# Kernel tuning notes

Hardware: AMD Instinct MI355X
Metric: run time of the kernel (lower is better)

Reference implementation:

```python
import jax, jax.numpy as jnp
import numpy as np

B, DE, T = 32, 256, 32
H, W, C = 128, 128, 128  # units == C


def setup_inputs() -> dict:
    key = jax.random.key(0)
    k1, k2, k3 = jax.random.split(key, 3)
    e = jax.random.normal(k1, (B, DE, T), dtype=jnp.float32)
    h = jax.random.normal(k2, (B, H, W, C), dtype=jnp.float32)
    Wd = jax.random.normal(k3, (DE, C), dtype=jnp.float32) * (1.0 / np.sqrt(DE))
    b = jnp.zeros((C,), dtype=jnp.float32)
    return {"e": e, "h": h, "Wd": Wd, "b": b}


def reference(e, h, Wd, b):
    # e: [B, DE, T]  -> dense over DE -> e_: [B, C, T]
    e_ = jnp.einsum('bdt,dc->bct', e, Wd) + b[None, :, None]
    Bh, Hh, Wh, Ch = h.shape
    HW = Hh * Wh
    # h NHWC -> [B, C, HW]
    h1 = h.transpose(0, 3, 1, 2).reshape(Bh, Ch, HW)
    # scores: [B, T, HW], contraction over channels
    s = jnp.einsum('bct,bcn->btn', e_, h1)
    # softmax over T (axis=1)
    beta = jax.nn.softmax(s, axis=1)
    # context: [B, C, HW]
    c = jnp.einsum('bct,btn->bcn', e_, beta)
    # -> [B, HW, C] -> NHWC
    c = c.transpose(0, 2, 1).reshape(Bh, Hh, Wh, Ch)
    return jnp.concatenate([c, h], axis=3)  # [B, H, W, 2C]
```

## Files before the change

kernel.cpp:

```cpp
#include <hip/hip_runtime.h>

typedef float v2f __attribute__((ext_vector_type(2)));

#define B_   32
#define DE_  256
#define T_   32
#define C_   128
#define HW_  16384

#define HSTRIDE 257

__device__ inline v2f vfma2(v2f a, v2f b, v2f c) {
#if __has_builtin(__builtin_elementwise_fma)
    return __builtin_elementwise_fma(a, b, c);
#else
    v2f r; r.x = fmaf(a.x, b.x, c.x); r.y = fmaf(a.y, b.y, c.y); return r;
#endif
}

__global__ __launch_bounds__(256) void dense_e_kernel(
    const float* __restrict__ e, const float* __restrict__ Wd,
    const float* __restrict__ bias, float* __restrict__ ews)
{
    __shared__ float elds[DE_ * T_];
    __shared__ float wlds[DE_ * 16];
    const int b   = blockIdx.y;
    const int cq  = blockIdx.x;
    const int tid = threadIdx.x;

    {
        const float4* erow = (const float4*)(e + ((size_t)b * DE_ + tid) * T_);
        float4* edst = (float4*)(elds + tid * T_);
        #pragma unroll
        for (int i = 0; i < 8; ++i) edst[i] = erow[i];

        const float4* wrow = (const float4*)(Wd + (size_t)tid * C_ + cq * 16);
        float4* wdst = (float4*)(wlds + tid * 16);
        #pragma unroll
        for (int i = 0; i < 4; ++i) wdst[i] = wrow[i];
    }
    __syncthreads();

    const int t  = tid & 31;
    const int c8 = tid >> 5;
    float a0 = 0.f, a1 = 0.f;
    #pragma unroll 8
    for (int d = 0; d < DE_; ++d) {
        float ev = elds[d * T_ + t];
        a0 = fmaf(ev, wlds[d * 16 + c8],     a0);
        a1 = fmaf(ev, wlds[d * 16 + 8 + c8], a1);
    }
    const int c0 = cq * 16 + c8;
    a0 += bias[c0];
    a1 += bias[c0 + 8];
    ews[((size_t)b * C_ + c0)     * T_ + t] = a0;
    ews[((size_t)b * C_ + c0 + 8) * T_ + t] = a1;
}

__global__ __launch_bounds__(128) void attn_fused_kernel(
    const float* __restrict__ h,
    const float* __restrict__ ews,
    float* __restrict__ out)
{
    __shared__ float hT[16 * HSTRIDE];
    __shared__ float es[16 * T_];

    const int b   = blockIdx.x >> 6;
    const int n0  = (blockIdx.x & 63) << 8;
    const int tid = threadIdx.x;
    const float* __restrict__ eb = ews + (size_t)b * (C_ * T_);
    const float* __restrict__ hb = h   + ((size_t)b * HW_ + n0) * C_;
    float* __restrict__       ob = out + ((size_t)b * HW_ + n0) * (2 * C_);

    v2f s0[16], s1[16];
    #pragma unroll
    for (int i = 0; i < 16; ++i) { s0[i] = (v2f){0.f, 0.f}; s1[i] = (v2f){0.f, 0.f}; }

    for (int ch = 0; ch < 8; ++ch) {
        float4 hv[8];
        #pragma unroll
        for (int i = 0; i < 8; ++i) {
            const int idx = i * 128 + tid;
            hv[i] = *(const float4*)(hb + (size_t)(idx >> 2) * C_ + ch * 16 + (idx & 3) * 4);
        }
        ((float4*)es)[tid] = ((const float4*)(eb + ch * 16 * T_))[tid];
        #pragma unroll
        for (int i = 0; i < 8; ++i) {
            const int idx = i * 128 + tid;
            const int row = idx >> 2, c4 = idx & 3;
            *(float4*)(ob + (size_t)row * (2 * C_) + C_ + ch * 16 + c4 * 4) = hv[i];
            float* d = hT + (c4 * 4) * HSTRIDE + row;
            d[0]           = hv[i].x;
            d[HSTRIDE]     = hv[i].y;
            d[2 * HSTRIDE] = hv[i].z;
            d[3 * HSTRIDE] = hv[i].w;
        }
        __syncthreads();

        #pragma unroll
        for (int cl = 0; cl < 16; ++cl) {
            const float h0 = hT[cl * HSTRIDE + tid];
            const float h1 = hT[cl * HSTRIDE + 128 + tid];
            const float4* ec4 = (const float4*)(es + cl * T_);
            const v2f h0v = {h0, h0}, h1v = {h1, h1};
            #pragma unroll
            for (int k = 0; k < 8; ++k) {
                const float4 ef = ec4[k];
                const v2f eA = {ef.x, ef.y}, eB = {ef.z, ef.w};
                s0[2 * k]     = vfma2(h0v, eA, s0[2 * k]);
                s0[2 * k + 1] = vfma2(h0v, eB, s0[2 * k + 1]);
                s1[2 * k]     = vfma2(h1v, eA, s1[2 * k]);
                s1[2 * k + 1] = vfma2(h1v, eB, s1[2 * k + 1]);
            }
        }
        __syncthreads();
    }

    {
        v2f m2 = s0[0];
        #pragma unroll
        for (int i = 1; i < 16; ++i) { m2.x = fmaxf(m2.x, s0[i].x); m2.y = fmaxf(m2.y, s0[i].y); }
        const float m = fmaxf(m2.x, m2.y);
        float l = 0.f;
        #pragma unroll
        for (int i = 0; i < 16; ++i) {
            v2f p; p.x = __expf(s0[i].x - m); p.y = __expf(s0[i].y - m);
            s0[i] = p; l += p.x + p.y;
        }
        const float inv = 1.0f / l;
        #pragma unroll
        for (int i = 0; i < 16; ++i) { s0[i].x *= inv; s0[i].y *= inv; }
    }
    {
        v2f m2 = s1[0];
        #pragma unroll
        for (int i = 1; i < 16; ++i) { m2.x = fmaxf(m2.x, s1[i].x); m2.y = fmaxf(m2.y, s1[i].y); }
        const float m = fmaxf(m2.x, m2.y);
        float l = 0.f;
        #pragma unroll
        for (int i = 0; i < 16; ++i) {
            v2f p; p.x = __expf(s1[i].x - m); p.y = __expf(s1[i].y - m);
            s1[i] = p; l += p.x + p.y;
        }
        const float inv = 1.0f / l;
        #pragma unroll
        for (int i = 0; i < 16; ++i) { s1[i].x *= inv; s1[i].y *= inv; }
    }

    for (int ch = 0; ch < 8; ++ch) {
        ((float4*)es)[tid] = ((const float4*)(eb + ch * 16 * T_))[tid];
        __syncthreads();
        #pragma unroll
        for (int cl = 0; cl < 16; ++cl) {
            const float4* ec4 = (const float4*)(es + cl * T_);
            v2f a0 = {0.f, 0.f}, a1 = {0.f, 0.f};
            #pragma unroll
            for (int k = 0; k < 8; ++k) {
                const float4 ef = ec4[k];
                const v2f eA = {ef.x, ef.y}, eB = {ef.z, ef.w};
                a0 = vfma2(eA, s0[2 * k], a0);
                a0 = vfma2(eB, s0[2 * k + 1], a0);
                a1 = vfma2(eA, s1[2 * k], a1);
                a1 = vfma2(eB, s1[2 * k + 1], a1);
            }
            hT[cl * HSTRIDE + tid]       = a0.x + a0.y;
            hT[cl * HSTRIDE + 128 + tid] = a1.x + a1.y;
        }
        __syncthreads();
        #pragma unroll
        for (int i = 0; i < 8; ++i) {
            const int idx = i * 128 + tid;
            const int row = idx >> 2, c4 = idx & 3;
            const float* src = hT + (c4 * 4) * HSTRIDE + row;
            float4 st = { src[0], src[HSTRIDE], src[2 * HSTRIDE], src[3 * HSTRIDE] };
            *(float4*)(ob + (size_t)row * (2 * C_) + ch * 16 + c4 * 4) = st;
        }
        __syncthreads();
    }
}

extern "C" void kernel_launch(void* const* d_in, const int* in_sizes, int n_in,
                              void* d_out, int out_size, void* d_ws, size_t ws_size,
                              hipStream_t stream) {
    const float* e    = (const float*)d_in[0];
    const float* h    = (const float*)d_in[1];
    const float* Wd   = (const float*)d_in[2];
    const float* bias = (const float*)d_in[3];
    float* ews = (float*)d_ws;
    float* out = (float*)d_out;

    dense_e_kernel<<<dim3(8, 32), 256, 0, stream>>>(e, Wd, bias, ews);
    attn_fused_kernel<<<dim3(32 * (HW_ / 256)), 128, 0, stream>>>(h, ews, out);
}
```

Measured before the change: 866.1 us.

## Software-pipeline h and e chunk loads with register prefetch and double-buffered LDS

Prefetches the next 16-channel chunk of h and the e slice into registers while computing scores on the current chunk. The e slices in shared memory are double-buffered, which removes one barrier per iteration in both the score and context loops. The aim is to hide global memory latency behind the FMA work. In exchange, more registers stay live (the hv[8] prefetch alongside 64 score accumulators), which may lower occupancy or cause spills.

```diff
diff --git a/kernel.cpp b/kernel.cpp
--- a/kernel.cpp
+++ b/kernel.cpp
@@ -63,7 +63,7 @@
     float* __restrict__ out)
 {
     __shared__ float hT[16 * HSTRIDE];
-    __shared__ float es[16 * T_];
+    __shared__ float es[2][16 * T_];
 
     const int b   = blockIdx.x >> 6;
     const int n0  = (blockIdx.x & 63) << 8;
@@ -76,32 +76,51 @@
     #pragma unroll
     for (int i = 0; i < 16; ++i) { s0[i] = (v2f){0.f, 0.f}; s1[i] = (v2f){0.f, 0.f}; }
 
+    float4 hv[8];
+    #pragma unroll
+    for (int i = 0; i < 8; ++i) {
+        const int idx = i * 128 + tid;
+        hv[i] = *(const float4*)(hb + (size_t)(idx >> 2) * C_ + (idx & 3) * 4);
+    }
+    float4 ereg = ((const float4*)(eb))[tid];
+
     for (int ch = 0; ch < 8; ++ch) {
-        float4 hv[8];
-        #pragma unroll
-        for (int i = 0; i < 8; ++i) {
-            const int idx = i * 128 + tid;
-            hv[i] = *(const float4*)(hb + (size_t)(idx >> 2) * C_ + ch * 16 + (idx & 3) * 4);
-        }
-        ((float4*)es)[tid] = ((const float4*)(eb + ch * 16 * T_))[tid];
+        if (ch) __syncthreads();
+
         #pragma unroll
         for (int i = 0; i < 8; ++i) {
             const int idx = i * 128 + tid;
             const int row = idx >> 2, c4 = idx & 3;
-            *(float4*)(ob + (size_t)row * (2 * C_) + C_ + ch * 16 + c4 * 4) = hv[i];
             float* d = hT + (c4 * 4) * HSTRIDE + row;
             d[0]           = hv[i].x;
             d[HSTRIDE]     = hv[i].y;
             d[2 * HSTRIDE] = hv[i].z;
             d[3 * HSTRIDE] = hv[i].w;
         }
+        ((float4*)es[ch & 1])[tid] = ereg;
         __syncthreads();
 
+        #pragma unroll
+        for (int i = 0; i < 8; ++i) {
+            const int idx = i * 128 + tid;
+            const int row = idx >> 2, c4 = idx & 3;
+            *(float4*)(ob + (size_t)row * (2 * C_) + C_ + ch * 16 + c4 * 4) = hv[i];
+        }
+        if (ch < 7) {
+            #pragma unroll
+            for (int i = 0; i < 8; ++i) {
+                const int idx = i * 128 + tid;
+                hv[i] = *(const float4*)(hb + (size_t)(idx >> 2) * C_ + (ch + 1) * 16 + (idx & 3) * 4);
+            }
+            ereg = ((const float4*)(eb + (ch + 1) * 16 * T_))[tid];
+        }
+
+        const float* esc = es[ch & 1];
         #pragma unroll
         for (int cl = 0; cl < 16; ++cl) {
             const float h0 = hT[cl * HSTRIDE + tid];
             const float h1 = hT[cl * HSTRIDE + 128 + tid];
-            const float4* ec4 = (const float4*)(es + cl * T_);
+            const float4* ec4 = (const float4*)(esc + cl * T_);
             const v2f h0v = {h0, h0}, h1v = {h1, h1};
             #pragma unroll
             for (int k = 0; k < 8; ++k) {
@@ -113,7 +132,6 @@
                 s1[2 * k + 1] = vfma2(h1v, eB, s1[2 * k + 1]);
             }
         }
-        __syncthreads();
     }
 
     {
@@ -147,12 +165,19 @@
         for (int i = 0; i < 16; ++i) { s1[i].x *= inv; s1[i].y *= inv; }
     }
 
+    float4 ep0 = ((const float4*)(eb))[tid];
+    float4 ep1 = ((const float4*)(eb + 16 * T_))[tid];
+    __syncthreads();
+    ((float4*)es[0])[tid] = ep0;
+    ((float4*)es[1])[tid] = ep1;
+    __syncthreads();
+    float4 epn = ((const float4*)(eb + 2 * 16 * T_))[tid];
+
     for (int ch = 0; ch < 8; ++ch) {
-        ((float4*)es)[tid] = ((const float4*)(eb + ch * 16 * T_))[tid];
-        __syncthreads();
+        const float* esc = es[ch & 1];
         #pragma unroll
         for (int cl = 0; cl < 16; ++cl) {
-            const float4* ec4 = (const float4*)(es + cl * T_);
+            const float4* ec4 = (const float4*)(esc + cl * T_);
             v2f a0 = {0.f, 0.f}, a1 = {0.f, 0.f};
             #pragma unroll
             for (int k = 0; k < 8; ++k) {
@@ -167,6 +192,8 @@
             hT[cl * HSTRIDE + 128 + tid] = a1.x + a1.y;
         }
         __syncthreads();
+        if (ch < 6) ((float4*)es[ch & 1])[tid] = epn;
+        if (ch < 5) epn = ((const float4*)(eb + (ch + 3) * 16 * T_))[tid];
         #pragma unroll
         for (int i = 0; i < 8; ++i) {
             const int idx = i * 128 + tid;
@@ -175,7 +202,7 @@
             float4 st = { src[0], src[HSTRIDE], src[2 * HSTRIDE], src[3 * HSTRIDE] };
             *(float4*)(ob + (size_t)row * (2 * C_) + ch * 16 + c4 * 4) = st;
         }
-        __syncthreads();
+        if (ch < 7) __syncthreads();
     }
 }
 
```

Result: faster. 836.0 us (-3.5%).
